# Optimization experiments

Hardware: AMD Instinct MI355X
Metric: run time of the kernel (lower is better)

The kernel has to match this reference:

```python
import jax, jax.numpy as jnp
import numpy as np
import math

D_MODEL = 768
NUM_HEADS = 12
SPARSITY = 0.7


def setup_inputs() -> dict:
    key = jax.random.key(0)
    ks = jax.random.split(key, 9)
    B, S, D = 2, 2048, D_MODEL
    scale = 1.0 / math.sqrt(D)  # xavier-ish
    inp = {
        "x": jax.random.normal(ks[0], (B, S, D), dtype=jnp.float32),
        "Wq": jax.random.normal(ks[1], (D, D), dtype=jnp.float32) * scale,
        "bq": jnp.zeros((D,), dtype=jnp.float32),
        "Wk": jax.random.normal(ks[2], (D, D), dtype=jnp.float32) * scale,
        "bk": jnp.zeros((D,), dtype=jnp.float32),
        "Wv": jax.random.normal(ks[3], (D, D), dtype=jnp.float32) * scale,
        "bv": jnp.zeros((D,), dtype=jnp.float32),
        "Wo": jax.random.normal(ks[4], (D, D), dtype=jnp.float32) * scale,
        "bo": jnp.zeros((D,), dtype=jnp.float32),
    }
    return inp


def reference(x, Wq, bq, Wk, bk, Wv, bv, Wo, bo):
    B, S, D = x.shape
    H = NUM_HEADS
    hd = D // H
    k_keep = max(1, int((1.0 - SPARSITY) * S))

    # projections (nn.Linear: x @ W.T + b), split into heads -> [B,H,S,hd]
    q = (x @ Wq.T + bq).reshape(B, S, H, hd).transpose(0, 2, 1, 3)
    k = (x @ Wk.T + bk).reshape(B, S, H, hd).transpose(0, 2, 1, 3)
    v = (x @ Wv.T + bv).reshape(B, S, H, hd).transpose(0, 2, 1, 3)

    # dense scores [B,H,S,S]
    scores = jnp.einsum("bhqd,bhkd->bhqk", q, k) / math.sqrt(hd)

    # per-row top-k sparsification (training path of the torch module)
    _, topk_idx = jax.lax.top_k(scores, k_keep)  # [B,H,S,k]
    bi = jnp.arange(B)[:, None, None, None]
    hi = jnp.arange(H)[None, :, None, None]
    si = jnp.arange(S)[None, None, :, None]
    keep = jnp.zeros(scores.shape, dtype=bool).at[bi, hi, si, topk_idx].set(True)
    scores = jnp.where(keep, scores, jnp.float32(-1e9))

    attn = jax.nn.softmax(scores, axis=-1)
    out = jnp.einsum("bhqk,bhkd->bhqd", attn, v)  # [B,H,S,hd]
    out = out.transpose(0, 2, 1, 3).reshape(B, S, D)
    return out @ Wo.T + bo
```

## Files before the change

### kernel.cpp

```cpp
#include <hip/hip_runtime.h>
#include <math.h>

#define B_ 2
#define S_ 2048
#define D_ 768
#define H_ 12
#define HD_ 64
#define KKEEP 614
#define M_ (B_*S_)
#define KD_ 768
#define SRW 2072

typedef __attribute__((ext_vector_type(8))) short bf8;
typedef __attribute__((ext_vector_type(4))) float f4;

__device__ __forceinline__ unsigned short f2bf(float f) {
    unsigned u = __float_as_uint(f);
    u += 0x7FFF + ((u >> 16) & 1);
    return (unsigned short)(u >> 16);
}
__device__ __forceinline__ float bf2f(unsigned short h) {
    return __uint_as_float((unsigned)h << 16);
}
__device__ __forceinline__ unsigned f2ord16(float f) {
    unsigned u = __float_as_uint(f);
    unsigned o32 = u ^ ((unsigned)((int)u >> 31) | 0x80000000u);
    return (o32 + 0x7FFFu + ((o32 >> 16) & 1u)) >> 16;
}
__device__ __forceinline__ float ord16_to_f(unsigned o16) {
    unsigned o = o16 << 16;
    unsigned mask = 0x80000000u | ~(unsigned)((int)o >> 31);
    return __uint_as_float((o ^ mask) & 0xFFFF0000u);
}
__device__ __forceinline__ void gl_lds16(const unsigned short* g, unsigned short* l) {
    __builtin_amdgcn_global_load_lds(
        (const __attribute__((address_space(1))) void*)g,
        (__attribute__((address_space(3))) void*)l, 16, 0, 0);
}

__global__ void split_all(const float* __restrict__ x,
                          const float* __restrict__ w0, const float* __restrict__ w1,
                          const float* __restrict__ w2, const float* __restrict__ w3,
                          unsigned short* __restrict__ xhi, unsigned short* __restrict__ xlo,
                          unsigned short* __restrict__ whi, unsigned short* __restrict__ wlo) {
    const int NPc = M_ * D_;
    const int NWc = D_ * D_;
    int i = blockIdx.x * blockDim.x + threadIdx.x;
    float f;
    unsigned short *ph, *pl;
    int o;
    if (i < NPc) {
        f = x[i]; ph = xhi; pl = xlo; o = i;
    } else {
        int j = i - NPc;
        int which = j / NWc;
        int k = j - which * NWc;
        const float* src = which == 0 ? w0 : which == 1 ? w1 : which == 2 ? w2 : w3;
        f = src[k]; ph = whi; pl = wlo; o = j;
    }
    unsigned short h = f2bf(f);
    ph[o] = h;
    pl[o] = f2bf(f - bf2f(h));
}

__global__ __launch_bounds__(256)
void gemm_qkv(const unsigned short* __restrict__ Ahi, const unsigned short* __restrict__ Alo,
              const unsigned short* __restrict__ Wch, const unsigned short* __restrict__ Wcl,
              const float* __restrict__ bq, const float* __restrict__ bk,
              const float* __restrict__ bv,
              unsigned short* __restrict__ Qh, unsigned short* __restrict__ Ql,
              unsigned short* __restrict__ Kh, unsigned short* __restrict__ Vth) {
    __shared__ __align__(16) unsigned short Ah[128][32], Al[128][32], Bh[64][32], Bl[64][32];
    const int bm = blockIdx.x * 128, bnG = blockIdx.y * 64;
    const int which = blockIdx.y / 12;
    const int bn = bnG - which * 768;
    const float* bias = which == 0 ? bq : (which == 1 ? bk : bv);
    const int tid = threadIdx.x, lane = tid & 63, wave = tid >> 6;
    const int col = lane & 15, quad = lane >> 4;

    f4 acc[2][4];
#pragma unroll
    for (int mi = 0; mi < 2; ++mi)
#pragma unroll
        for (int ni = 0; ni < 4; ++ni) { f4 z = {0.f,0.f,0.f,0.f}; acc[mi][ni] = z; }

    for (int kt = 0; kt < KD_; kt += 32) {
        __syncthreads();
#pragma unroll
        for (int c = 0; c < 2; ++c) {
            int idx = c * 256 + tid;
            int row = idx >> 2, ko = (idx & 3) * 8;
            gl_lds16(&Ahi[(size_t)(bm + row) * KD_ + kt + ko], &Ah[0][0] + idx * 8);
            gl_lds16(&Alo[(size_t)(bm + row) * KD_ + kt + ko], &Al[0][0] + idx * 8);
        }
        {
            int row = tid >> 2, ko = (tid & 3) * 8;
            gl_lds16(&Wch[(size_t)(bnG + row) * KD_ + kt + ko], &Bh[0][0] + tid * 8);
            gl_lds16(&Wcl[(size_t)(bnG + row) * KD_ + kt + ko], &Bl[0][0] + tid * 8);
        }
        __syncthreads();

        bf8 af[2][2], wf[4][2];
#pragma unroll
        for (int mi = 0; mi < 2; ++mi) {
            int r = wave * 32 + mi * 16 + col;
            af[mi][0] = *(const bf8*)&Ah[r][quad * 8];
            af[mi][1] = *(const bf8*)&Al[r][quad * 8];
        }
#pragma unroll
        for (int ni = 0; ni < 4; ++ni) {
            int r = ni * 16 + col;
            wf[ni][0] = *(const bf8*)&Bh[r][quad * 8];
            wf[ni][1] = *(const bf8*)&Bl[r][quad * 8];
        }
#pragma unroll
        for (int mi = 0; mi < 2; ++mi)
#pragma unroll
            for (int ni = 0; ni < 4; ++ni) {
                acc[mi][ni] = __builtin_amdgcn_mfma_f32_16x16x32_bf16(af[mi][0], wf[ni][0], acc[mi][ni], 0, 0, 0);
                acc[mi][ni] = __builtin_amdgcn_mfma_f32_16x16x32_bf16(af[mi][1], wf[ni][0], acc[mi][ni], 0, 0, 0);
                acc[mi][ni] = __builtin_amdgcn_mfma_f32_16x16x32_bf16(af[mi][0], wf[ni][1], acc[mi][ni], 0, 0, 0);
            }
    }

    float bvv[4];
#pragma unroll
    for (int ni = 0; ni < 4; ++ni) bvv[ni] = bias[bn + ni * 16 + col];
#pragma unroll
    for (int mi = 0; mi < 2; ++mi)
#pragma unroll
        for (int ni = 0; ni < 4; ++ni)
#pragma unroll
            for (int r = 0; r < 4; ++r) {
                int m = bm + wave * 32 + mi * 16 + quad * 4 + r;
                int n = bn + ni * 16 + col;
                float v = acc[mi][ni][r] + bvv[ni];
                if (which == 0) v *= 0.125f;
                int b = m >> 11, s = m & 2047, h = n >> 6, d = n & 63;
                unsigned short hh = f2bf(v);
                if (which == 0) {
                    size_t idx = (((size_t)b * H_ + h) * S_ + s) * HD_ + d;
                    Qh[idx] = hh;
                    Ql[idx] = f2bf(v - bf2f(hh));
                } else if (which == 1) {
                    Kh[(((size_t)b * H_ + h) * S_ + s) * HD_ + d] = hh;
                } else {
                    Vth[(((size_t)b * H_ + h) * HD_ + d) * S_ + s] = hh;
                }
            }
}

__global__ __launch_bounds__(256)
void gemm_o(const unsigned short* __restrict__ Ahi, const unsigned short* __restrict__ Alo,
            const unsigned short* __restrict__ Whi, const unsigned short* __restrict__ Wlo,
            const float* __restrict__ bias, float* __restrict__ outf) {
    __shared__ __align__(16) unsigned short Ah[128][32], Al[128][32], Bh[64][32], Bl[64][32];
    const int bm = blockIdx.x * 128, bn = blockIdx.y * 64;
    const int tid = threadIdx.x, lane = tid & 63, wave = tid >> 6;
    const int col = lane & 15, quad = lane >> 4;

    f4 acc[2][4];
#pragma unroll
    for (int mi = 0; mi < 2; ++mi)
#pragma unroll
        for (int ni = 0; ni < 4; ++ni) { f4 z = {0.f,0.f,0.f,0.f}; acc[mi][ni] = z; }

    for (int kt = 0; kt < KD_; kt += 32) {
        __syncthreads();
#pragma unroll
        for (int c = 0; c < 2; ++c) {
            int idx = c * 256 + tid;
            int row = idx >> 2, ko = (idx & 3) * 8;
            gl_lds16(&Ahi[(size_t)(bm + row) * KD_ + kt + ko], &Ah[0][0] + idx * 8);
            gl_lds16(&Alo[(size_t)(bm + row) * KD_ + kt + ko], &Al[0][0] + idx * 8);
        }
        {
            int row = tid >> 2, ko = (tid & 3) * 8;
            gl_lds16(&Whi[(size_t)(bn + row) * KD_ + kt + ko], &Bh[0][0] + tid * 8);
            gl_lds16(&Wlo[(size_t)(bn + row) * KD_ + kt + ko], &Bl[0][0] + tid * 8);
        }
        __syncthreads();

        bf8 af[2][2], wf[4][2];
#pragma unroll
        for (int mi = 0; mi < 2; ++mi) {
            int r = wave * 32 + mi * 16 + col;
            af[mi][0] = *(const bf8*)&Ah[r][quad * 8];
            af[mi][1] = *(const bf8*)&Al[r][quad * 8];
        }
#pragma unroll
        for (int ni = 0; ni < 4; ++ni) {
            int r = ni * 16 + col;
            wf[ni][0] = *(const bf8*)&Bh[r][quad * 8];
            wf[ni][1] = *(const bf8*)&Bl[r][quad * 8];
        }
#pragma unroll
        for (int mi = 0; mi < 2; ++mi)
#pragma unroll
            for (int ni = 0; ni < 4; ++ni) {
                acc[mi][ni] = __builtin_amdgcn_mfma_f32_16x16x32_bf16(af[mi][0], wf[ni][0], acc[mi][ni], 0, 0, 0);
                acc[mi][ni] = __builtin_amdgcn_mfma_f32_16x16x32_bf16(af[mi][1], wf[ni][0], acc[mi][ni], 0, 0, 0);
                acc[mi][ni] = __builtin_amdgcn_mfma_f32_16x16x32_bf16(af[mi][0], wf[ni][1], acc[mi][ni], 0, 0, 0);
            }
    }

    float bvv[4];
#pragma unroll
    for (int ni = 0; ni < 4; ++ni) bvv[ni] = bias[bn + ni * 16 + col];
#pragma unroll
    for (int mi = 0; mi < 2; ++mi)
#pragma unroll
        for (int ni = 0; ni < 4; ++ni)
#pragma unroll
            for (int r = 0; r < 4; ++r) {
                int m = bm + wave * 32 + mi * 16 + quad * 4 + r;
                int n = bn + ni * 16 + col;
                outf[(size_t)m * D_ + n] = acc[mi][ni][r] + bvv[ni];
            }
}

__global__ __launch_bounds__(1024, 8)
void attn_kernel(const unsigned short* __restrict__ Qhi, const unsigned short* __restrict__ Qlo,
                 const unsigned short* __restrict__ Khi,
                 const unsigned short* __restrict__ Vthi,
                 unsigned short* __restrict__ AOhi, unsigned short* __restrict__ AOlo) {
    const int bid = blockIdx.x;
    const int xcd = bid & 7, sub = (bid >> 3) % 3, tile = bid / 24;
    const int bh = xcd * 3 + sub;
    const int b = bh / H_, h = bh % H_;
    const int q0 = tile * 16;
    const int tid = threadIdx.x, lane = tid & 63, wave = tid >> 6;
    const int col = lane & 15, quad = lane >> 4;

    __shared__ __align__(16) unsigned char arena[16 * 4144];
    unsigned short* scB = (unsigned short*)arena;
    float (*osum)[16][64] = (float (*)[16][64])arena;
    __shared__ float linv[16];

    const size_t qbase = ((size_t)bh * S_ + q0 + col) * HD_;
    bf8 qh0 = *(const bf8*)&Qhi[qbase + quad * 8];
    bf8 qh1 = *(const bf8*)&Qhi[qbase + 32 + quad * 8];
    bf8 ql0 = *(const bf8*)&Qlo[qbase + quad * 8];
    bf8 ql1 = *(const bf8*)&Qlo[qbase + 32 + quad * 8];

    const size_t kbb = (size_t)bh * S_ * HD_;
#pragma unroll 1
    for (int t = 0; t < 8; ++t) {
        const size_t kr = kbb + (size_t)(wave * 128 + t * 16 + col) * HD_;
        bf8 kh0 = *(const bf8*)&Khi[kr + quad * 8];
        bf8 kh1 = *(const bf8*)&Khi[kr + 32 + quad * 8];
        f4 a = {0.f, 0.f, 0.f, 0.f};
        a = __builtin_amdgcn_mfma_f32_16x16x32_bf16(qh0, kh0, a, 0, 0, 0);
        a = __builtin_amdgcn_mfma_f32_16x16x32_bf16(qh1, kh1, a, 0, 0, 0);
        a = __builtin_amdgcn_mfma_f32_16x16x32_bf16(ql0, kh0, a, 0, 0, 0);
        a = __builtin_amdgcn_mfma_f32_16x16x32_bf16(ql1, kh1, a, 0, 0, 0);
#pragma unroll
        for (int r = 0; r < 4; ++r)
            scB[(quad * 4 + r) * SRW + wave * 128 + t * 16 + col] =
                (unsigned short)f2ord16(a[r]);
    }
    __syncthreads();

    unsigned* rowp = (unsigned*)(arena + wave * 4144);
    unsigned kv[16], kvs[16];
#pragma unroll
    for (int j = 0; j < 16; ++j) kv[j] = rowp[lane + 64 * j];
#pragma unroll
    for (int j = 0; j < 16; ++j) kvs[j] = kv[j] << 16;

    unsigned Mhi = 0, Mlo = 0;
#pragma unroll
    for (int j = 0; j < 16; ++j) {
        Mhi = kv[j]  > Mhi ? kv[j]  : Mhi;
        Mlo = kvs[j] > Mlo ? kvs[j] : Mlo;
    }
    unsigned mo = (Mhi >> 16) > (Mlo >> 16) ? (Mhi >> 16) : (Mlo >> 16);
#pragma unroll
    for (int off = 1; off < 64; off <<= 1) {
        unsigned v = __shfl_xor((int)mo, off, 64);
        mo = mo > v ? mo : v;
    }

    unsigned T = 0;
#pragma unroll 1
    for (int bit = 15; bit >= 0; --bit) {
        unsigned candh = (T | (1u << bit)) << 16;
        int cnt = 0;
#pragma unroll
        for (int j = 0; j < 16; ++j) {
            cnt += __popcll(__ballot(kv[j]  >= candh));
            cnt += __popcll(__ballot(kvs[j] >= candh));
        }
        if (cnt >= KKEEP) {
            T |= (1u << bit);
            if (cnt == KKEEP) break;
        }
    }

    const float L2E = 1.44269504f;
    const float mb = ord16_to_f(mo) * L2E;
    float ls = 0.f;
#pragma unroll 1
    for (int j = 0; j < 16; ++j) {
        unsigned lo16 = kv[j] & 0xFFFFu;
        unsigned hi16 = kv[j] >> 16;
        float wl = __builtin_amdgcn_exp2f(__builtin_fmaf(ord16_to_f(lo16), L2E, -mb));
        float wh = __builtin_amdgcn_exp2f(__builtin_fmaf(ord16_to_f(hi16), L2E, -mb));
        wl = (lo16 >= T) ? wl : 0.f;
        wh = (hi16 >= T) ? wh : 0.f;
        ls += wl + wh;
        rowp[lane + 64 * j] = (unsigned)f2bf(wl) | ((unsigned)f2bf(wh) << 16);
    }
#pragma unroll
    for (int off = 1; off < 64; off <<= 1) ls += __shfl_xor(ls, off, 64);
    if (lane == 0) linv[wave] = 1.f / ls;
    __syncthreads();

    f4 od[4];
#pragma unroll
    for (int dt = 0; dt < 4; ++dt) { f4 z = {0.f,0.f,0.f,0.f}; od[dt] = z; }
    const size_t vbb = (size_t)bh * HD_ * S_;
#pragma unroll 1
    for (int c = 0; c < 4; ++c) {
        bf8 ph = *(const bf8*)&scB[col * SRW + wave * 128 + c * 32 + quad * 8];
        const size_t sbase = (size_t)(wave * 128 + c * 32 + quad * 8);
#pragma unroll
        for (int dt = 0; dt < 4; ++dt) {
            bf8 vh = *(const bf8*)&Vthi[vbb + (size_t)(dt * 16 + col) * S_ + sbase];
            od[dt] = __builtin_amdgcn_mfma_f32_16x16x32_bf16(ph, vh, od[dt], 0, 0, 0);
        }
    }
    __syncthreads();
#pragma unroll
    for (int dt = 0; dt < 4; ++dt)
#pragma unroll
        for (int r = 0; r < 4; ++r)
            osum[wave][quad * 4 + r][dt * 16 + col] = od[dt][r];
    __syncthreads();

    {
        int q = tid >> 6, d = tid & 63;
        float s = 0.f;
#pragma unroll
        for (int w = 0; w < 16; ++w) s += osum[w][q][d];
        s *= linv[q];
        size_t idx = ((size_t)b * S_ + q0 + q) * D_ + h * HD_ + d;
        unsigned short hh = f2bf(s);
        AOhi[idx] = hh;
        AOlo[idx] = f2bf(s - bf2f(hh));
    }
}

extern "C" void kernel_launch(void* const* d_in, const int* in_sizes, int n_in,
                              void* d_out, int out_size, void* d_ws, size_t ws_size,
                              hipStream_t stream) {
    const float* x  = (const float*)d_in[0];
    const float* Wq = (const float*)d_in[1];
    const float* bq = (const float*)d_in[2];
    const float* Wk = (const float*)d_in[3];
    const float* bk = (const float*)d_in[4];
    const float* Wv = (const float*)d_in[5];
    const float* bv = (const float*)d_in[6];
    const float* Wo = (const float*)d_in[7];
    const float* bo = (const float*)d_in[8];
    float* out = (float*)d_out;

    const size_t NP = (size_t)M_ * D_;
    const size_t NW = (size_t)D_ * D_;
    unsigned short* p = (unsigned short*)d_ws;
    unsigned short* xhi = p;  p += NP;
    unsigned short* xlo = p;  p += NP;
    unsigned short* Wch = p;  p += 4 * NW;
    unsigned short* Wcl = p;  p += 4 * NW;
    unsigned short* Qh  = p;  p += NP;  unsigned short* Ql  = p;  p += NP;
    unsigned short* Kh  = p;  p += NP;
    unsigned short* Vth = p;  p += NP;
    unsigned short* AOh = xhi;
    unsigned short* AOl = xlo;

    {
        int total = (int)(NP + 4 * NW);
        split_all<<<total / 256, 256, 0, stream>>>(x, Wq, Wk, Wv, Wo,
                                                   xhi, xlo, Wch, Wcl);
    }

    {
        dim3 g(M_ / 128, 36);
        gemm_qkv<<<g, 256, 0, stream>>>(xhi, xlo, Wch, Wcl, bq, bk, bv,
                                        Qh, Ql, Kh, Vth);
    }

    attn_kernel<<<(S_ / 16) * B_ * H_, 1024, 0, stream>>>(Qh, Ql, Kh, Vth, AOh, AOl);

    {
        dim3 g(M_ / 128, D_ / 64);
        gemm_o<<<g, 256, 0, stream>>>(AOh, AOl, Wch + 3 * NW, Wcl + 3 * NW, bo, out);
    }
}
```

Baseline: 432.5 us.

## Drop weight low-part split in GEMMs and halve attention query tile

The weight matrices are now rounded to a single bf16 part, so the QKV and output GEMMs issue two MFMAs per tile instead of three and no longer load a low-part weight tile. The split kernel stops writing a low-part weight buffer. The attention kernel now handles 8 query rows per block with 512 threads instead of 16 with 1024. Each wave covers 256 keys, and only half the MFMA output rows are kept, since rows 8-15 duplicate rows 0-7. This trades some weight precision and MFMA utilisation in attention for more blocks, smaller LDS per block and less GEMM work.

```diff
diff --git a/kernel.cpp b/kernel.cpp
--- a/kernel.cpp
+++ b/kernel.cpp
@@ -10,6 +10,7 @@
 #define M_ (B_*S_)
 #define KD_ 768
 #define SRW 2072
+#define TQ 8
 
 typedef __attribute__((ext_vector_type(8))) short bf8;
 typedef __attribute__((ext_vector_type(4))) float f4;
@@ -42,35 +43,32 @@
                           const float* __restrict__ w0, const float* __restrict__ w1,
                           const float* __restrict__ w2, const float* __restrict__ w3,
                           unsigned short* __restrict__ xhi, unsigned short* __restrict__ xlo,
-                          unsigned short* __restrict__ whi, unsigned short* __restrict__ wlo) {
+                          unsigned short* __restrict__ whi) {
     const int NPc = M_ * D_;
     const int NWc = D_ * D_;
     int i = blockIdx.x * blockDim.x + threadIdx.x;
-    float f;
-    unsigned short *ph, *pl;
-    int o;
     if (i < NPc) {
-        f = x[i]; ph = xhi; pl = xlo; o = i;
+        float f = x[i];
+        unsigned short h = f2bf(f);
+        xhi[i] = h;
+        xlo[i] = f2bf(f - bf2f(h));
     } else {
         int j = i - NPc;
         int which = j / NWc;
         int k = j - which * NWc;
         const float* src = which == 0 ? w0 : which == 1 ? w1 : which == 2 ? w2 : w3;
-        f = src[k]; ph = whi; pl = wlo; o = j;
-    }
-    unsigned short h = f2bf(f);
-    ph[o] = h;
-    pl[o] = f2bf(f - bf2f(h));
+        whi[j] = f2bf(src[k]);
+    }
 }
 
 __global__ __launch_bounds__(256)
 void gemm_qkv(const unsigned short* __restrict__ Ahi, const unsigned short* __restrict__ Alo,
-              const unsigned short* __restrict__ Wch, const unsigned short* __restrict__ Wcl,
+              const unsigned short* __restrict__ Wch,
               const float* __restrict__ bq, const float* __restrict__ bk,
               const float* __restrict__ bv,
               unsigned short* __restrict__ Qh, unsigned short* __restrict__ Ql,
               unsigned short* __restrict__ Kh, unsigned short* __restrict__ Vth) {
-    __shared__ __align__(16) unsigned short Ah[128][32], Al[128][32], Bh[64][32], Bl[64][32];
+    __shared__ __align__(16) unsigned short Ah[128][32], Al[128][32], Bh[64][32];
     const int bm = blockIdx.x * 128, bnG = blockIdx.y * 64;
     const int which = blockIdx.y / 12;
     const int bn = bnG - which * 768;
@@ -96,11 +94,10 @@
         {
             int row = tid >> 2, ko = (tid & 3) * 8;
             gl_lds16(&Wch[(size_t)(bnG + row) * KD_ + kt + ko], &Bh[0][0] + tid * 8);
-            gl_lds16(&Wcl[(size_t)(bnG + row) * KD_ + kt + ko], &Bl[0][0] + tid * 8);
         }
         __syncthreads();
 
-        bf8 af[2][2], wf[4][2];
+        bf8 af[2][2], wf[4];
 #pragma unroll
         for (int mi = 0; mi < 2; ++mi) {
             int r = wave * 32 + mi * 16 + col;
@@ -108,18 +105,14 @@
             af[mi][1] = *(const bf8*)&Al[r][quad * 8];
         }
 #pragma unroll
-        for (int ni = 0; ni < 4; ++ni) {
-            int r = ni * 16 + col;
-            wf[ni][0] = *(const bf8*)&Bh[r][quad * 8];
-            wf[ni][1] = *(const bf8*)&Bl[r][quad * 8];
-        }
+        for (int ni = 0; ni < 4; ++ni)
+            wf[ni] = *(const bf8*)&Bh[ni * 16 + col][quad * 8];
 #pragma unroll
         for (int mi = 0; mi < 2; ++mi)
 #pragma unroll
             for (int ni = 0; ni < 4; ++ni) {
-                acc[mi][ni] = __builtin_amdgcn_mfma_f32_16x16x32_bf16(af[mi][0], wf[ni][0], acc[mi][ni], 0, 0, 0);
-                acc[mi][ni] = __builtin_amdgcn_mfma_f32_16x16x32_bf16(af[mi][1], wf[ni][0], acc[mi][ni], 0, 0, 0);
-                acc[mi][ni] = __builtin_amdgcn_mfma_f32_16x16x32_bf16(af[mi][0], wf[ni][1], acc[mi][ni], 0, 0, 0);
+                acc[mi][ni] = __builtin_amdgcn_mfma_f32_16x16x32_bf16(af[mi][0], wf[ni], acc[mi][ni], 0, 0, 0);
+                acc[mi][ni] = __builtin_amdgcn_mfma_f32_16x16x32_bf16(af[mi][1], wf[ni], acc[mi][ni], 0, 0, 0);
             }
     }
 
@@ -152,9 +145,9 @@
 
 __global__ __launch_bounds__(256)
 void gemm_o(const unsigned short* __restrict__ Ahi, const unsigned short* __restrict__ Alo,
-            const unsigned short* __restrict__ Whi, const unsigned short* __restrict__ Wlo,
+            const unsigned short* __restrict__ Whi,
             const float* __restrict__ bias, float* __restrict__ outf) {
-    __shared__ __align__(16) unsigned short Ah[128][32], Al[128][32], Bh[64][32], Bl[64][32];
+    __shared__ __align__(16) unsigned short Ah[128][32], Al[128][32], Bh[64][32];
     const int bm = blockIdx.x * 128, bn = blockIdx.y * 64;
     const int tid = threadIdx.x, lane = tid & 63, wave = tid >> 6;
     const int col = lane & 15, quad = lane >> 4;
@@ -177,11 +170,10 @@
         {
             int row = tid >> 2, ko = (tid & 3) * 8;
             gl_lds16(&Whi[(size_t)(bn + row) * KD_ + kt + ko], &Bh[0][0] + tid * 8);
-            gl_lds16(&Wlo[(size_t)(bn + row) * KD_ + kt + ko], &Bl[0][0] + tid * 8);
         }
         __syncthreads();
 
-        bf8 af[2][2], wf[4][2];
+        bf8 af[2][2], wf[4];
 #pragma unroll
         for (int mi = 0; mi < 2; ++mi) {
             int r = wave * 32 + mi * 16 + col;
@@ -189,18 +181,14 @@
             af[mi][1] = *(const bf8*)&Al[r][quad * 8];
         }
 #pragma unroll
-        for (int ni = 0; ni < 4; ++ni) {
-            int r = ni * 16 + col;
-            wf[ni][0] = *(const bf8*)&Bh[r][quad * 8];
-            wf[ni][1] = *(const bf8*)&Bl[r][quad * 8];
-        }
+        for (int ni = 0; ni < 4; ++ni)
+            wf[ni] = *(const bf8*)&Bh[ni * 16 + col][quad * 8];
 #pragma unroll
         for (int mi = 0; mi < 2; ++mi)
 #pragma unroll
             for (int ni = 0; ni < 4; ++ni) {
-                acc[mi][ni] = __builtin_amdgcn_mfma_f32_16x16x32_bf16(af[mi][0], wf[ni][0], acc[mi][ni], 0, 0, 0);
-                acc[mi][ni] = __builtin_amdgcn_mfma_f32_16x16x32_bf16(af[mi][1], wf[ni][0], acc[mi][ni], 0, 0, 0);
-                acc[mi][ni] = __builtin_amdgcn_mfma_f32_16x16x32_bf16(af[mi][0], wf[ni][1], acc[mi][ni], 0, 0, 0);
+                acc[mi][ni] = __builtin_amdgcn_mfma_f32_16x16x32_bf16(af[mi][0], wf[ni], acc[mi][ni], 0, 0, 0);
+                acc[mi][ni] = __builtin_amdgcn_mfma_f32_16x16x32_bf16(af[mi][1], wf[ni], acc[mi][ni], 0, 0, 0);
             }
     }
 
@@ -219,7 +207,7 @@
             }
 }
 
-__global__ __launch_bounds__(1024, 8)
+__global__ __launch_bounds__(512, 8)
 void attn_kernel(const unsigned short* __restrict__ Qhi, const unsigned short* __restrict__ Qlo,
                  const unsigned short* __restrict__ Khi,
                  const unsigned short* __restrict__ Vthi,
@@ -228,16 +216,16 @@
     const int xcd = bid & 7, sub = (bid >> 3) % 3, tile = bid / 24;
     const int bh = xcd * 3 + sub;
     const int b = bh / H_, h = bh % H_;
-    const int q0 = tile * 16;
+    const int q0 = tile * TQ;
     const int tid = threadIdx.x, lane = tid & 63, wave = tid >> 6;
     const int col = lane & 15, quad = lane >> 4;
 
-    __shared__ __align__(16) unsigned char arena[16 * 4144];
+    __shared__ __align__(16) unsigned char arena[TQ * 4144];
     unsigned short* scB = (unsigned short*)arena;
-    float (*osum)[16][64] = (float (*)[16][64])arena;
-    __shared__ float linv[16];
-
-    const size_t qbase = ((size_t)bh * S_ + q0 + col) * HD_;
+    float (*osum)[TQ][64] = (float (*)[TQ][64])arena;
+    __shared__ float linv[TQ];
+
+    const size_t qbase = ((size_t)bh * S_ + q0 + (col & 7)) * HD_;
     bf8 qh0 = *(const bf8*)&Qhi[qbase + quad * 8];
     bf8 qh1 = *(const bf8*)&Qhi[qbase + 32 + quad * 8];
     bf8 ql0 = *(const bf8*)&Qlo[qbase + quad * 8];
@@ -245,8 +233,9 @@
 
     const size_t kbb = (size_t)bh * S_ * HD_;
 #pragma unroll 1
-    for (int t = 0; t < 8; ++t) {
-        const size_t kr = kbb + (size_t)(wave * 128 + t * 16 + col) * HD_;
+    for (int t = 0; t < 16; ++t) {
+        const int key = wave * 256 + t * 16 + col;
+        const size_t kr = kbb + (size_t)key * HD_;
         bf8 kh0 = *(const bf8*)&Khi[kr + quad * 8];
         bf8 kh1 = *(const bf8*)&Khi[kr + 32 + quad * 8];
         f4 a = {0.f, 0.f, 0.f, 0.f};
@@ -254,10 +243,11 @@
         a = __builtin_amdgcn_mfma_f32_16x16x32_bf16(qh1, kh1, a, 0, 0, 0);
         a = __builtin_amdgcn_mfma_f32_16x16x32_bf16(ql0, kh0, a, 0, 0, 0);
         a = __builtin_amdgcn_mfma_f32_16x16x32_bf16(ql1, kh1, a, 0, 0, 0);
-#pragma unroll
-        for (int r = 0; r < 4; ++r)
-            scB[(quad * 4 + r) * SRW + wave * 128 + t * 16 + col] =
-                (unsigned short)f2ord16(a[r]);
+        if (quad < 2) {
+#pragma unroll
+            for (int r = 0; r < 4; ++r)
+                scB[(quad * 4 + r) * SRW + key] = (unsigned short)f2ord16(a[r]);
+        }
     }
     __syncthreads();
 
@@ -321,9 +311,9 @@
     for (int dt = 0; dt < 4; ++dt) { f4 z = {0.f,0.f,0.f,0.f}; od[dt] = z; }
     const size_t vbb = (size_t)bh * HD_ * S_;
 #pragma unroll 1
-    for (int c = 0; c < 4; ++c) {
-        bf8 ph = *(const bf8*)&scB[col * SRW + wave * 128 + c * 32 + quad * 8];
-        const size_t sbase = (size_t)(wave * 128 + c * 32 + quad * 8);
+    for (int c = 0; c < 8; ++c) {
+        const int sbase = wave * 256 + c * 32 + quad * 8;
+        bf8 ph = *(const bf8*)&scB[(col & 7) * SRW + sbase];
 #pragma unroll
         for (int dt = 0; dt < 4; ++dt) {
             bf8 vh = *(const bf8*)&Vthi[vbb + (size_t)(dt * 16 + col) * S_ + sbase];
@@ -331,18 +321,20 @@
         }
     }
     __syncthreads();
-#pragma unroll
-    for (int dt = 0; dt < 4; ++dt)
-#pragma unroll
-        for (int r = 0; r < 4; ++r)
-            osum[wave][quad * 4 + r][dt * 16 + col] = od[dt][r];
+    if (quad < 2) {
+#pragma unroll
+        for (int dt = 0; dt < 4; ++dt)
+#pragma unroll
+            for (int r = 0; r < 4; ++r)
+                osum[wave][quad * 4 + r][dt * 16 + col] = od[dt][r];
+    }
     __syncthreads();
 
     {
         int q = tid >> 6, d = tid & 63;
         float s = 0.f;
 #pragma unroll
-        for (int w = 0; w < 16; ++w) s += osum[w][q][d];
+        for (int w = 0; w < 8; ++w) s += osum[w][q][d];
         s *= linv[q];
         size_t idx = ((size_t)b * S_ + q0 + q) * D_ + h * HD_ + d;
         unsigned short hh = f2bf(s);
@@ -371,7 +363,6 @@
     unsigned short* xhi = p;  p += NP;
     unsigned short* xlo = p;  p += NP;
     unsigned short* Wch = p;  p += 4 * NW;
-    unsigned short* Wcl = p;  p += 4 * NW;
     unsigned short* Qh  = p;  p += NP;  unsigned short* Ql  = p;  p += NP;
     unsigned short* Kh  = p;  p += NP;
     unsigned short* Vth = p;  p += NP;
@@ -380,20 +371,18 @@
 
     {
         int total = (int)(NP + 4 * NW);
-        split_all<<<total / 256, 256, 0, stream>>>(x, Wq, Wk, Wv, Wo,
-                                                   xhi, xlo, Wch, Wcl);
+        split_all<<<total / 256, 256, 0, stream>>>(x, Wq, Wk, Wv, Wo, xhi, xlo, Wch);
     }
 
     {
         dim3 g(M_ / 128, 36);
-        gemm_qkv<<<g, 256, 0, stream>>>(xhi, xlo, Wch, Wcl, bq, bk, bv,
-                                        Qh, Ql, Kh, Vth);
-    }
-
-    attn_kernel<<<(S_ / 16) * B_ * H_, 1024, 0, stream>>>(Qh, Ql, Kh, Vth, AOh, AOl);
+        gemm_qkv<<<g, 256, 0, stream>>>(xhi, xlo, Wch, bq, bk, bv, Qh, Ql, Kh, Vth);
+    }
+
+    attn_kernel<<<(S_ / TQ) * B_ * H_, 512, 0, stream>>>(Qh, Ql, Kh, Vth, AOh, AOl);
 
     {
         dim3 g(M_ / 128, D_ / 64);
-        gemm_o<<<g, 256, 0, stream>>>(AOh, AOl, Wch + 3 * NW, Wcl + 3 * NW, bo, out);
-    }
-}
+        gemm_o<<<g, 256, 0, stream>>>(AOh, AOl, Wch + 3 * NW, bo, out);
+    }
+}
```

After: 529.0 us. 22.3% more time.
